# Kernel tuning notes

Hardware: AMD Instinct MI355X
Metric: run time of the kernel (lower is better)

Reference implementation:

```python
import jax, jax.numpy as jnp
import numpy as np

T, B, H, L = 200, 32, 1024, 2
DROPOUT = 0.32
KEEP = 1.0 - DROPOUT
FORGET_GATE_BIAS = 1.0


def setup_inputs() -> dict:
    key = jax.random.key(0)
    ks = jax.random.split(key, 8)
    scale = 1.0 / np.sqrt(H)  # torch LSTM default init: U(-1/sqrt(H), 1/sqrt(H))
    x = jax.random.normal(ks[0], (T, B, H), jnp.float32)
    W_ih = jax.random.uniform(ks[1], (L, 4 * H, H), jnp.float32, -scale, scale)
    W_hh = jax.random.uniform(ks[2], (L, 4 * H, H), jnp.float32, -scale, scale)
    b_ih = jax.random.uniform(ks[3], (L, 4 * H), jnp.float32, -scale, scale)
    b_hh = jax.random.uniform(ks[4], (L, 4 * H), jnp.float32, -scale, scale)
    # forget-gate bias init as in LstmDrop.__init__ (gate order i,f,g,o)
    b_ih = b_ih.at[:, H:2 * H].set(FORGET_GATE_BIAS)
    b_hh = b_hh.at[:, H:2 * H].set(0.0)
    h0 = jnp.zeros((L, B, H), jnp.float32)
    c0 = jnp.zeros((L, B, H), jnp.float32)
    # inverted dropout masks: inter-layer (torch LSTM dropout, applied to all but last layer)
    # and the trailing inplace Dropout on the output sequence
    mask_inter = (jax.random.bernoulli(ks[5], KEEP, (L - 1, T, B, H)) / KEEP).astype(jnp.float32)
    mask_out = (jax.random.bernoulli(ks[6], KEEP, (T, B, H)) / KEEP).astype(jnp.float32)
    return {"x": x, "h0": h0, "c0": c0, "W_ih": W_ih, "W_hh": W_hh,
            "b_ih": b_ih, "b_hh": b_hh, "mask_inter": mask_inter, "mask_out": mask_out}


def _lstm_layer(xs, h, c, Wih, Whh, b):
    # xs: [T,B,in]; Wih/Whh: [4H,in]/[4H,H]; b: [4H] (b_ih + b_hh fused)
    def step(carry, x_t):
        h, c = carry
        gates = x_t @ Wih.T + h @ Whh.T + b  # [B,4H]
        i, f, g, o = jnp.split(gates, 4, axis=-1)
        c = jax.nn.sigmoid(f) * c + jax.nn.sigmoid(i) * jnp.tanh(g)
        h = jax.nn.sigmoid(o) * jnp.tanh(c)
        return (h, c), h
    (hT, cT), ys = jax.lax.scan(step, (h, c), xs)
    return ys, hT, cT


def reference(x, h0, c0, W_ih, W_hh, b_ih, b_hh, mask_inter, mask_out):
    y = x
    h_last, c_last = [], []
    for l in range(L):
        y, hT, cT = _lstm_layer(y, h0[l], c0[l], W_ih[l], W_hh[l], b_ih[l] + b_hh[l])
        h_last.append(hT)
        c_last.append(cT)
        if l < L - 1:  # torch LSTM applies dropout between layers only
            y = y * mask_inter[l]
    y = y * mask_out  # the inplace Dropout on the output sequence
    return y, jnp.stack(h_last), jnp.stack(c_last)
```

## Files before the change

kernel.cpp:

```cpp
#include <hip/hip_runtime.h>

#define T_STEPS 200
#define BATCH   32
#define HID     1024
#define NWG     256
#define NTHR    512

typedef _Float16 half8 __attribute__((ext_vector_type(8)));
typedef float    f32x4 __attribute__((ext_vector_type(4)));

__device__ __forceinline__ half8 ld_coh16(const _Float16* p) {
    union { unsigned long long u[2]; half8 h; } r;
    const unsigned long long* q = (const unsigned long long*)p;
    r.u[0] = __hip_atomic_load(q,     __ATOMIC_RELAXED, __HIP_MEMORY_SCOPE_AGENT);
    r.u[1] = __hip_atomic_load(q + 1, __ATOMIC_RELAXED, __HIP_MEMORY_SCOPE_AGENT);
    return r.h;
}
__device__ __forceinline__ void st_coh16(_Float16* p, half8 v) {
    union { half8 h; unsigned long long u[2]; } r; r.h = v;
    unsigned long long* q = (unsigned long long*)p;
    __hip_atomic_store(q,     r.u[0], __ATOMIC_RELAXED, __HIP_MEMORY_SCOPE_AGENT);
    __hip_atomic_store(q + 1, r.u[1], __ATOMIC_RELAXED, __HIP_MEMORY_SCOPE_AGENT);
}

__device__ __forceinline__ half8 cvt8(const float* p) {
    f32x4 lo = *(const f32x4*)p;
    f32x4 hi = *(const f32x4*)(p + 4);
    half8 a;
    a[0] = (_Float16)lo[0]; a[1] = (_Float16)lo[1];
    a[2] = (_Float16)lo[2]; a[3] = (_Float16)lo[3];
    a[4] = (_Float16)hi[0]; a[5] = (_Float16)hi[1];
    a[6] = (_Float16)hi[2]; a[7] = (_Float16)hi[3];
    return a;
}

__global__ void init_k(const float* __restrict__ h0,
                       _Float16* __restrict__ h0b, _Float16* __restrict__ h1b,
                       unsigned* __restrict__ flag0, unsigned* __restrict__ flag1) {
    int i = blockIdx.x * blockDim.x + threadIdx.x;
    if (i < BATCH * HID) {
        h0b[i] = (_Float16)h0[i];
        h1b[i] = (_Float16)h0[BATCH * HID + i];
    }
    if (blockIdx.x == 0) {
        if (threadIdx.x < 128)      flag0[threadIdx.x * 32] = 0;
        else if (threadIdx.x < 256) flag1[(threadIdx.x - 128) * 32] = 0;
    }
}

__global__ __launch_bounds__(NTHR, 2) void lstm_main(
    const float* __restrict__ x, const float* __restrict__ c0,
    const float* __restrict__ Wih, const float* __restrict__ Whh,
    const float* __restrict__ bih, const float* __restrict__ bhh,
    const float* __restrict__ mi, const float* __restrict__ mo,
    float* __restrict__ out,
    _Float16* __restrict__ y0m, _Float16* __restrict__ h0b,
    _Float16* __restrict__ h1b, unsigned* __restrict__ flag0,
    unsigned* __restrict__ flag1)
{
    __shared__ _Float16 W_s[32 * 2048];
    __shared__ float scr[8][2][16][17];
    __shared__ float c_s[BATCH][8];
    __shared__ alignas(16) _Float16 st_h[BATCH][8];
    __shared__ alignas(16) _Float16 st_y[BATCH][8];
    __shared__ float st_o[BATCH][8];

    const int bid   = blockIdx.x;
    const int layer = bid >> 7;
    const int wgl   = bid & 127;
    const int tid   = threadIdx.x;

    const float* WihL = Wih + (size_t)layer * 4 * HID * HID;
    const float* WhhL = Whh + (size_t)layer * 4 * HID * HID;
    for (int idx = tid; idx < 32 * 2048; idx += NTHR) {
        int r = idx >> 11, k = idx & 2047;
        int grow = (r >> 3) * HID + wgl * 8 + (r & 7);
        float v = (k < HID) ? WihL[(size_t)grow * HID + k]
                            : WhhL[(size_t)grow * HID + (k - HID)];
        W_s[idx ^ ((r & 7) << 3)] = (_Float16)v;
    }

    float bias0 = 0.f, bias1 = 0.f, bias2 = 0.f, bias3 = 0.f;
    int b_ = 0, col_ = 0, gcol = 0;
    if (tid < 256) {
        b_ = tid >> 3; col_ = tid & 7; gcol = wgl * 8 + col_;
        bias0 = bih[layer * 4096 + gcol]           + bhh[layer * 4096 + gcol];
        bias1 = bih[layer * 4096 + HID + gcol]     + bhh[layer * 4096 + HID + gcol];
        bias2 = bih[layer * 4096 + 2 * HID + gcol] + bhh[layer * 4096 + 2 * HID + gcol];
        bias3 = bih[layer * 4096 + 3 * HID + gcol] + bhh[layer * 4096 + 3 * HID + gcol];
        c_s[b_][col_] = c0[((size_t)layer * BATCH + b_) * HID + gcol];
    }
    const int ot = tid - 256;
    const int b2 = (ot >= 0) ? (ot >> 3) : 0, c2 = (ot >= 0) ? (ot & 7) : 0;
    const int gcol2 = wgl * 8 + c2;
    __syncthreads();

    const int lane = tid & 63, wid = tid >> 6;
    int kq;
    if (layer == 0) kq = (wid < 4) ? (2 + (wid >> 1)) : ((wid - 4) >> 1);
    else            kq = wid >> 1;
    const int mm   = wid & 1;
    const int srow = kq * 2 + mm;
    const int row = lane & 15, bb = mm * 16 + row, ko = (lane >> 4) * 8;

    half8 aF[16];
    float mi_reg = 0.f, mo_reg = 0.f;
    if (layer == 0 && kq < 2) {
        const float* xp = x + (size_t)bb * HID + kq * 512 + ko;
        #pragma unroll
        for (int kk = 0; kk < 16; ++kk) aF[kk] = cvt8(xp + kk * 32);
    }
    if (layer == 1 && ot >= 0) mo_reg = mo[(size_t)b2 * HID + gcol2];

    for (int s = 0; s < T_STEPS; ++s) {
        if (layer == 0) {
            if (tid < 128) {
                const unsigned* f = flag0 + tid * 32;
                const unsigned tgt = (unsigned)s;
                while (__hip_atomic_load(f, __ATOMIC_RELAXED,
                                         __HIP_MEMORY_SCOPE_AGENT) < tgt) {}
            }
        } else {
            if (tid < 128) {
                const unsigned* f = flag0 + tid * 32;
                const unsigned tgt = (unsigned)(s + 1);
                while (__hip_atomic_load(f, __ATOMIC_RELAXED,
                                         __HIP_MEMORY_SCOPE_AGENT) < tgt) {}
            } else if (tid < 256) {
                const unsigned* f = flag1 + (tid - 128) * 32;
                const unsigned tgt = (unsigned)s;
                while (__hip_atomic_load(f, __ATOMIC_RELAXED,
                                         __HIP_MEMORY_SCOPE_AGENT) < tgt) {}
            }
        }
        asm volatile("" ::: "memory");
        __syncthreads();

        if (layer == 0 && tid < 256)
            mi_reg = mi[((size_t)s * BATCH + b_) * HID + gcol];

        if (layer == 0) {
            if (kq >= 2) {
                const _Float16* hp = h0b + (s & 1) * (BATCH * HID)
                                   + bb * HID + (kq - 2) * 512 + ko;
                #pragma unroll
                for (int kk = 0; kk < 16; ++kk) aF[kk] = ld_coh16(hp + kk * 32);
            }
        } else {
            if (kq < 2) {
                const _Float16* yp = y0m + ((size_t)s * BATCH + bb) * HID + kq * 512 + ko;
                #pragma unroll
                for (int kk = 0; kk < 16; ++kk) aF[kk] = ld_coh16(yp + kk * 32);
            } else {
                const _Float16* hp = h1b + (s & 1) * (BATCH * HID)
                                   + bb * HID + (kq - 2) * 512 + ko;
                #pragma unroll
                for (int kk = 0; kk < 16; ++kk) aF[kk] = ld_coh16(hp + kk * 32);
            }
        }

        f32x4 acc0 = {0.f, 0.f, 0.f, 0.f}, acc1 = {0.f, 0.f, 0.f, 0.f};
        #pragma unroll
        for (int kk = 0; kk < 16; ++kk) {
            const int k  = kq * 512 + kk * 32 + ko;
            const int r1 = 16 + row;
            const half8 bB0 = *(const half8*)&W_s[(row * 2048 + k) ^ ((row & 7) << 3)];
            const half8 bB1 = *(const half8*)&W_s[(r1 * 2048 + k) ^ ((r1 & 7) << 3)];
            acc0 = __builtin_amdgcn_mfma_f32_16x16x32_f16(aF[kk], bB0, acc0, 0, 0, 0);
            acc1 = __builtin_amdgcn_mfma_f32_16x16x32_f16(aF[kk], bB1, acc1, 0, 0, 0);
        }
        #pragma unroll
        for (int j = 0; j < 4; ++j) {
            scr[srow][0][(lane >> 4) * 4 + j][row] = acc0[j];
            scr[srow][1][(lane >> 4) * 4 + j][row] = acc1[j];
        }
        __syncthreads();

        if (tid < 256) {
            const int m2 = b_ >> 4, rD = b_ & 15;
            float v0 = 0.f, v1 = 0.f, v2 = 0.f, v3 = 0.f;
            #pragma unroll
            for (int q = 0; q < 4; ++q) {
                v0 += scr[q * 2 + m2][0][rD][col_];
                v1 += scr[q * 2 + m2][0][rD][8 + col_];
                v2 += scr[q * 2 + m2][1][rD][col_];
                v3 += scr[q * 2 + m2][1][rD][8 + col_];
            }
            const float ig = 1.f / (1.f + __expf(-(v0 + bias0)));
            const float fg = 1.f / (1.f + __expf(-(v1 + bias1)));
            const float gg = tanhf(v2 + bias2);
            const float og = 1.f / (1.f + __expf(-(v3 + bias3)));
            const float cc = fg * c_s[b_][col_] + ig * gg;
            const float hh = og * tanhf(cc);
            c_s[b_][col_] = cc;

            st_h[b_][col_] = (_Float16)hh;
            if (layer == 0) st_y[b_][col_] = (_Float16)(hh * mi_reg);
            else            st_o[b_][col_] = hh;

            if (s == T_STEPS - 1) {
                const size_t base = (size_t)T_STEPS * BATCH * HID;
                out[base + ((size_t)layer * BATCH + b_) * HID + gcol] = hh;
                out[base + (size_t)2 * BATCH * HID + ((size_t)layer * BATCH + b_) * HID + gcol] = cc;
            }
        }
        __syncthreads();

        if (layer == 0) {
            if (wid >= 4) {
                if (tid >= 448 && tid < 480) {
                    const int sl = tid - 448;
                    st_coh16(&h0b[((s + 1) & 1) * (BATCH * HID) + sl * HID + wgl * 8],
                             *(const half8*)st_h[sl]);
                    st_coh16(&y0m[((size_t)s * BATCH + sl) * HID + wgl * 8],
                             *(const half8*)st_y[sl]);
                    asm volatile("s_waitcnt vmcnt(0)" ::: "memory");
                    if (tid == 448)
                        __hip_atomic_store(flag0 + wgl * 32, (unsigned)(s + 1),
                                           __ATOMIC_RELAXED, __HIP_MEMORY_SCOPE_AGENT);
                }
                if (kq < 2 && s + 1 < T_STEPS) {
                    const float* xp = x + ((size_t)(s + 1) * BATCH + bb) * HID + kq * 512 + ko;
                    #pragma unroll
                    for (int kk = 0; kk < 16; ++kk) aF[kk] = cvt8(xp + kk * 32);
                }
            }
        } else {
            if (ot >= 0) {
                out[((size_t)s * BATCH + b2) * HID + gcol2] = st_o[b2][c2] * mo_reg;
                if (tid >= 448 && tid < 480) {
                    const int sl = tid - 448;
                    st_coh16(&h1b[((s + 1) & 1) * (BATCH * HID) + sl * HID + wgl * 8],
                             *(const half8*)st_h[sl]);
                    asm volatile("s_waitcnt vmcnt(0)" ::: "memory");
                    if (tid == 448)
                        __hip_atomic_store(flag1 + wgl * 32, (unsigned)(s + 1),
                                           __ATOMIC_RELAXED, __HIP_MEMORY_SCOPE_AGENT);
                }
                if (s + 1 < T_STEPS)
                    mo_reg = mo[((size_t)(s + 1) * BATCH + b2) * HID + gcol2];
            }
        }
    }
}

extern "C" void kernel_launch(void* const* d_in, const int* in_sizes, int n_in,
                              void* d_out, int out_size, void* d_ws, size_t ws_size,
                              hipStream_t stream) {
    const float* x   = (const float*)d_in[0];
    const float* h0  = (const float*)d_in[1];
    const float* c0  = (const float*)d_in[2];
    const float* Wih = (const float*)d_in[3];
    const float* Whh = (const float*)d_in[4];
    const float* bih = (const float*)d_in[5];
    const float* bhh = (const float*)d_in[6];
    const float* mi  = (const float*)d_in[7];
    const float* mo  = (const float*)d_in[8];
    float* out = (float*)d_out;

    char* w = (char*)d_ws;
    _Float16* y0m   = (_Float16*)w;
    _Float16* h0b   = (_Float16*)(w + 13107200);
    _Float16* h1b   = (_Float16*)(w + 13107200 + 131072);
    unsigned* flag0 = (unsigned*)(w + 13107200 + 262144);
    unsigned* flag1 = (unsigned*)(w + 13107200 + 262144 + 16384);

    hipLaunchKernelGGL(init_k, dim3(128), dim3(256), 0, stream,
                       h0, h0b, h1b, flag0, flag1);

    void* args[] = {(void*)&x, (void*)&c0, (void*)&Wih, (void*)&Whh,
                    (void*)&bih, (void*)&bhh, (void*)&mi, (void*)&mo,
                    (void*)&out, (void*)&y0m, (void*)&h0b, (void*)&h1b,
                    (void*)&flag0, (void*)&flag1};
    hipLaunchCooperativeKernel((void*)lstm_main, dim3(NWG), dim3(NTHR),
                               args, 0, stream);
}
```

Before: 2.170 ms.

## Replace per-step flag barriers with tagged hidden-state words for dataflow sync

```diff
diff --git a/kernel.cpp b/kernel.cpp
--- a/kernel.cpp
+++ b/kernel.cpp
@@ -5,22 +5,25 @@
 #define HID     1024
 #define NWG     256
 #define NTHR    512
+#define HB      (BATCH * HID)
 
 typedef _Float16 half8 __attribute__((ext_vector_type(8)));
 typedef float    f32x4 __attribute__((ext_vector_type(4)));
-
-__device__ __forceinline__ half8 ld_coh16(const _Float16* p) {
-    union { unsigned long long u[2]; half8 h; } r;
-    const unsigned long long* q = (const unsigned long long*)p;
-    r.u[0] = __hip_atomic_load(q,     __ATOMIC_RELAXED, __HIP_MEMORY_SCOPE_AGENT);
-    r.u[1] = __hip_atomic_load(q + 1, __ATOMIC_RELAXED, __HIP_MEMORY_SCOPE_AGENT);
-    return r.h;
-}
+typedef unsigned long long u64;
+
+#define RLX __ATOMIC_RELAXED
+#define AGT __HIP_MEMORY_SCOPE_AGENT
+#define TAGMASK 0xFFFF0000FFFF0000ull
+
+static __device__ __forceinline__ unsigned short f16bits(_Float16 v) {
+    union { _Float16 f; unsigned short u; } c; c.f = v; return c.u;
+}
+
 __device__ __forceinline__ void st_coh16(_Float16* p, half8 v) {
-    union { half8 h; unsigned long long u[2]; } r; r.h = v;
-    unsigned long long* q = (unsigned long long*)p;
-    __hip_atomic_store(q,     r.u[0], __ATOMIC_RELAXED, __HIP_MEMORY_SCOPE_AGENT);
-    __hip_atomic_store(q + 1, r.u[1], __ATOMIC_RELAXED, __HIP_MEMORY_SCOPE_AGENT);
+    union { half8 h; u64 u[2]; } r; r.h = v;
+    u64* q = (u64*)p;
+    __hip_atomic_store(q,     r.u[0], RLX, AGT);
+    __hip_atomic_store(q + 1, r.u[1], RLX, AGT);
 }
 
 __device__ __forceinline__ half8 cvt8(const float* p) {
@@ -35,17 +38,16 @@
 }
 
 __global__ void init_k(const float* __restrict__ h0,
-                       _Float16* __restrict__ h0b, _Float16* __restrict__ h1b,
-                       unsigned* __restrict__ flag0, unsigned* __restrict__ flag1) {
+                       unsigned* __restrict__ h0w, unsigned* __restrict__ h1w,
+                       unsigned* __restrict__ flag0) {
     int i = blockIdx.x * blockDim.x + threadIdx.x;
-    if (i < BATCH * HID) {
-        h0b[i] = (_Float16)h0[i];
-        h1b[i] = (_Float16)h0[BATCH * HID + i];
-    }
-    if (blockIdx.x == 0) {
-        if (threadIdx.x < 128)      flag0[threadIdx.x * 32] = 0;
-        else if (threadIdx.x < 256) flag1[(threadIdx.x - 128) * 32] = 0;
-    }
+    if (i < HB) {
+        h0w[i]      = (1u << 16) | f16bits((_Float16)h0[i]);
+        h0w[HB + i] = 0u;
+        h1w[i]      = (1u << 16) | f16bits((_Float16)h0[HB + i]);
+        h1w[HB + i] = 0u;
+    }
+    if (blockIdx.x == 0 && threadIdx.x < 128) flag0[threadIdx.x * 32] = 0u;
 }
 
 __global__ __launch_bounds__(NTHR, 2) void lstm_main(
@@ -54,15 +56,14 @@
     const float* __restrict__ bih, const float* __restrict__ bhh,
     const float* __restrict__ mi, const float* __restrict__ mo,
     float* __restrict__ out,
-    _Float16* __restrict__ y0m, _Float16* __restrict__ h0b,
-    _Float16* __restrict__ h1b, unsigned* __restrict__ flag0,
-    unsigned* __restrict__ flag1)
+    _Float16* __restrict__ y0m, unsigned* __restrict__ h0w,
+    unsigned* __restrict__ h1w, unsigned* __restrict__ flag0)
 {
     __shared__ _Float16 W_s[32 * 2048];
     __shared__ float scr[8][2][16][17];
     __shared__ float c_s[BATCH][8];
-    __shared__ alignas(16) _Float16 st_h[BATCH][8];
     __shared__ alignas(16) _Float16 st_y[BATCH][8];
+    __shared__ float st_mi[BATCH][8];
     __shared__ float st_o[BATCH][8];
 
     const int bid   = blockIdx.x;
@@ -93,6 +94,10 @@
     const int ot = tid - 256;
     const int b2 = (ot >= 0) ? (ot >> 3) : 0, c2 = (ot >= 0) ? (ot & 7) : 0;
     const int gcol2 = wgl * 8 + c2;
+
+    float mo_reg = 0.f;
+    if (layer == 0 && ot >= 0) st_mi[b2][c2] = mi[(size_t)b2 * HID + gcol2];
+    if (layer == 1 && ot >= 0) mo_reg = mo[(size_t)b2 * HID + gcol2];
     __syncthreads();
 
     const int lane = tid & 63, wid = tid >> 6;
@@ -104,71 +109,78 @@
     const int row = lane & 15, bb = mm * 16 + row, ko = (lane >> 4) * 8;
 
     half8 aF[16];
-    float mi_reg = 0.f, mo_reg = 0.f;
     if (layer == 0 && kq < 2) {
         const float* xp = x + (size_t)bb * HID + kq * 512 + ko;
         #pragma unroll
         for (int kk = 0; kk < 16; ++kk) aF[kk] = cvt8(xp + kk * 32);
     }
-    if (layer == 1 && ot >= 0) mo_reg = mo[(size_t)b2 * HID + gcol2];
 
     for (int s = 0; s < T_STEPS; ++s) {
-        if (layer == 0) {
-            if (tid < 128) {
-                const unsigned* f = flag0 + tid * 32;
-                const unsigned tgt = (unsigned)s;
-                while (__hip_atomic_load(f, __ATOMIC_RELAXED,
-                                         __HIP_MEMORY_SCOPE_AGENT) < tgt) {}
+        f32x4 acc0 = {0.f, 0.f, 0.f, 0.f}, acc1 = {0.f, 0.f, 0.f, 0.f};
+
+        if (kq >= 2) {
+            const unsigned* __restrict__ hsrc = (layer == 0) ? h0w : h1w;
+            const unsigned tg = (unsigned)(s + 1);
+            const u64 expect = ((u64)tg << 48) | ((u64)tg << 16);
+            const unsigned* basew = hsrc + (s & 1) * HB + bb * HID + (kq - 2) * 512 + ko;
+            #pragma unroll
+            for (int c = 0; c < 4; ++c) {
+                u64 w[16];
+                #pragma unroll
+                for (int i = 0; i < 16; ++i)
+                    w[i] = __hip_atomic_load(
+                        (const u64*)(basew + (c * 4 + (i >> 2)) * 32 + (i & 3) * 2), RLX, AGT);
+                for (;;) {
+                    u64 bad = 0;
+                    #pragma unroll
+                    for (int i = 0; i < 16; ++i) bad |= (w[i] & TAGMASK) ^ expect;
+                    if (__all(bad == 0)) break;
+                    #pragma unroll
+                    for (int i = 0; i < 16; ++i)
+                        w[i] = __hip_atomic_load(
+                            (const u64*)(basew + (c * 4 + (i >> 2)) * 32 + (i & 3) * 2), RLX, AGT);
+                }
+                #pragma unroll
+                for (int k2 = 0; k2 < 4; ++k2) {
+                    union { half8 h; unsigned short u[8]; } a;
+                    #pragma unroll
+                    for (int j = 0; j < 8; ++j)
+                        a.u[j] = (unsigned short)(w[k2 * 4 + (j >> 1)] >> (32 * (j & 1)));
+                    const int kk = c * 4 + k2;
+                    const int k  = kq * 512 + kk * 32 + ko;
+                    const int r1 = 16 + row;
+                    const half8 bB0 = *(const half8*)&W_s[(row * 2048 + k) ^ ((row & 7) << 3)];
+                    const half8 bB1 = *(const half8*)&W_s[(r1 * 2048 + k) ^ ((r1 & 7) << 3)];
+                    acc0 = __builtin_amdgcn_mfma_f32_16x16x32_f16(a.h, bB0, acc0, 0, 0, 0);
+                    acc1 = __builtin_amdgcn_mfma_f32_16x16x32_f16(a.h, bB1, acc1, 0, 0, 0);
+                }
             }
         } else {
-            if (tid < 128) {
-                const unsigned* f = flag0 + tid * 32;
+            if (layer == 1) {
                 const unsigned tgt = (unsigned)(s + 1);
-                while (__hip_atomic_load(f, __ATOMIC_RELAXED,
-                                         __HIP_MEMORY_SCOPE_AGENT) < tgt) {}
-            } else if (tid < 256) {
-                const unsigned* f = flag1 + (tid - 128) * 32;
-                const unsigned tgt = (unsigned)s;
-                while (__hip_atomic_load(f, __ATOMIC_RELAXED,
-                                         __HIP_MEMORY_SCOPE_AGENT) < tgt) {}
-            }
-        }
-        asm volatile("" ::: "memory");
-        __syncthreads();
-
-        if (layer == 0 && tid < 256)
-            mi_reg = mi[((size_t)s * BATCH + b_) * HID + gcol];
-
-        if (layer == 0) {
-            if (kq >= 2) {
-                const _Float16* hp = h0b + (s & 1) * (BATCH * HID)
-                                   + bb * HID + (kq - 2) * 512 + ko;
-                #pragma unroll
-                for (int kk = 0; kk < 16; ++kk) aF[kk] = ld_coh16(hp + kk * 32);
-            }
-        } else {
-            if (kq < 2) {
+                const unsigned* fa = flag0 + (lane * 2) * 32;
+                const unsigned* fb = flag0 + (lane * 2 + 1) * 32;
+                for (;;) {
+                    unsigned va = __hip_atomic_load(fa, RLX, AGT);
+                    unsigned vb = __hip_atomic_load(fb, RLX, AGT);
+                    if (__all((va >= tgt) & (vb >= tgt))) break;
+                }
+                asm volatile("" ::: "memory");
                 const _Float16* yp = y0m + ((size_t)s * BATCH + bb) * HID + kq * 512 + ko;
                 #pragma unroll
-                for (int kk = 0; kk < 16; ++kk) aF[kk] = ld_coh16(yp + kk * 32);
-            } else {
-                const _Float16* hp = h1b + (s & 1) * (BATCH * HID)
-                                   + bb * HID + (kq - 2) * 512 + ko;
-                #pragma unroll
-                for (int kk = 0; kk < 16; ++kk) aF[kk] = ld_coh16(hp + kk * 32);
-            }
-        }
-
-        f32x4 acc0 = {0.f, 0.f, 0.f, 0.f}, acc1 = {0.f, 0.f, 0.f, 0.f};
-        #pragma unroll
-        for (int kk = 0; kk < 16; ++kk) {
-            const int k  = kq * 512 + kk * 32 + ko;
-            const int r1 = 16 + row;
-            const half8 bB0 = *(const half8*)&W_s[(row * 2048 + k) ^ ((row & 7) << 3)];
-            const half8 bB1 = *(const half8*)&W_s[(r1 * 2048 + k) ^ ((r1 & 7) << 3)];
-            acc0 = __builtin_amdgcn_mfma_f32_16x16x32_f16(aF[kk], bB0, acc0, 0, 0, 0);
-            acc1 = __builtin_amdgcn_mfma_f32_16x16x32_f16(aF[kk], bB1, acc1, 0, 0, 0);
-        }
+                for (int kk = 0; kk < 16; ++kk) aF[kk] = *(const half8*)(yp + kk * 32);
+            }
+            #pragma unroll
+            for (int kk = 0; kk < 16; ++kk) {
+                const int k  = kq * 512 + kk * 32 + ko;
+                const int r1 = 16 + row;
+                const half8 bB0 = *(const half8*)&W_s[(row * 2048 + k) ^ ((row & 7) << 3)];
+                const half8 bB1 = *(const half8*)&W_s[(r1 * 2048 + k) ^ ((r1 & 7) << 3)];
+                acc0 = __builtin_amdgcn_mfma_f32_16x16x32_f16(aF[kk], bB0, acc0, 0, 0, 0);
+                acc1 = __builtin_amdgcn_mfma_f32_16x16x32_f16(aF[kk], bB1, acc1, 0, 0, 0);
+            }
+        }
+
         #pragma unroll
         for (int j = 0; j < 4; ++j) {
             scr[srow][0][(lane >> 4) * 4 + j][row] = acc0[j];
@@ -194,49 +206,45 @@
             const float hh = og * tanhf(cc);
             c_s[b_][col_] = cc;
 
-            st_h[b_][col_] = (_Float16)hh;
-            if (layer == 0) st_y[b_][col_] = (_Float16)(hh * mi_reg);
-            else            st_o[b_][col_] = hh;
-
+            const unsigned hwrd = ((unsigned)(s + 2) << 16)
+                                | (unsigned)f16bits((_Float16)hh);
+            if (layer == 0) {
+                __hip_atomic_store(h0w + ((s + 1) & 1) * HB + b_ * HID + gcol,
+                                   hwrd, RLX, AGT);
+                st_y[b_][col_] = (_Float16)(hh * st_mi[b_][col_]);
+            } else {
+                __hip_atomic_store(h1w + ((s + 1) & 1) * HB + b_ * HID + gcol,
+                                   hwrd, RLX, AGT);
+                st_o[b_][col_] = hh;
+            }
             if (s == T_STEPS - 1) {
                 const size_t base = (size_t)T_STEPS * BATCH * HID;
                 out[base + ((size_t)layer * BATCH + b_) * HID + gcol] = hh;
-                out[base + (size_t)2 * BATCH * HID + ((size_t)layer * BATCH + b_) * HID + gcol] = cc;
+                out[base + (size_t)2 * BATCH * HID
+                    + ((size_t)layer * BATCH + b_) * HID + gcol] = cc;
             }
         }
         __syncthreads();
 
         if (layer == 0) {
-            if (wid >= 4) {
-                if (tid >= 448 && tid < 480) {
-                    const int sl = tid - 448;
-                    st_coh16(&h0b[((s + 1) & 1) * (BATCH * HID) + sl * HID + wgl * 8],
-                             *(const half8*)st_h[sl]);
-                    st_coh16(&y0m[((size_t)s * BATCH + sl) * HID + wgl * 8],
-                             *(const half8*)st_y[sl]);
-                    asm volatile("s_waitcnt vmcnt(0)" ::: "memory");
-                    if (tid == 448)
-                        __hip_atomic_store(flag0 + wgl * 32, (unsigned)(s + 1),
-                                           __ATOMIC_RELAXED, __HIP_MEMORY_SCOPE_AGENT);
-                }
-                if (kq < 2 && s + 1 < T_STEPS) {
-                    const float* xp = x + ((size_t)(s + 1) * BATCH + bb) * HID + kq * 512 + ko;
-                    #pragma unroll
-                    for (int kk = 0; kk < 16; ++kk) aF[kk] = cvt8(xp + kk * 32);
-                }
+            if (tid >= 448 && tid < 480) {
+                const int sl = tid - 448;
+                st_coh16(&y0m[((size_t)s * BATCH + sl) * HID + wgl * 8],
+                         *(const half8*)st_y[sl]);
+                asm volatile("s_waitcnt vmcnt(0)" ::: "memory");
+                if (tid == 448)
+                    __hip_atomic_store(flag0 + wgl * 32, (unsigned)(s + 1), RLX, AGT);
+            }
+            if (ot >= 0 && s + 1 < T_STEPS)
+                st_mi[b2][c2] = mi[((size_t)(s + 1) * BATCH + b2) * HID + gcol2];
+            if (wid >= 4 && kq < 2 && s + 1 < T_STEPS) {
+                const float* xp = x + ((size_t)(s + 1) * BATCH + bb) * HID + kq * 512 + ko;
+                #pragma unroll
+                for (int kk = 0; kk < 16; ++kk) aF[kk] = cvt8(xp + kk * 32);
             }
         } else {
             if (ot >= 0) {
                 out[((size_t)s * BATCH + b2) * HID + gcol2] = st_o[b2][c2] * mo_reg;
-                if (tid >= 448 && tid < 480) {
-                    const int sl = tid - 448;
-                    st_coh16(&h1b[((s + 1) & 1) * (BATCH * HID) + sl * HID + wgl * 8],
-                             *(const half8*)st_h[sl]);
-                    asm volatile("s_waitcnt vmcnt(0)" ::: "memory");
-                    if (tid == 448)
-                        __hip_atomic_store(flag1 + wgl * 32, (unsigned)(s + 1),
-                                           __ATOMIC_RELAXED, __HIP_MEMORY_SCOPE_AGENT);
-                }
                 if (s + 1 < T_STEPS)
                     mo_reg = mo[((size_t)(s + 1) * BATCH + b2) * HID + gcol2];
             }
@@ -260,18 +268,16 @@
 
     char* w = (char*)d_ws;
     _Float16* y0m   = (_Float16*)w;
-    _Float16* h0b   = (_Float16*)(w + 13107200);
-    _Float16* h1b   = (_Float16*)(w + 13107200 + 131072);
-    unsigned* flag0 = (unsigned*)(w + 13107200 + 262144);
-    unsigned* flag1 = (unsigned*)(w + 13107200 + 262144 + 16384);
-
-    hipLaunchKernelGGL(init_k, dim3(128), dim3(256), 0, stream,
-                       h0, h0b, h1b, flag0, flag1);
+    unsigned* h0w   = (unsigned*)(w + 13107200);
+    unsigned* h1w   = (unsigned*)(w + 13107200 + 262144);
+    unsigned* flag0 = (unsigned*)(w + 13107200 + 524288);
+
+    hipLaunchKernelGGL(init_k, dim3(128), dim3(256), 0, stream, h0, h0w, h1w, flag0);
 
     void* args[] = {(void*)&x, (void*)&c0, (void*)&Wih, (void*)&Whh,
                     (void*)&bih, (void*)&bhh, (void*)&mi, (void*)&mo,
-                    (void*)&out, (void*)&y0m, (void*)&h0b, (void*)&h1b,
-                    (void*)&flag0, (void*)&flag1};
+                    (void*)&out, (void*)&y0m, (void*)&h0w, (void*)&h1w,
+                    (void*)&flag0};
     hipLaunchCooperativeKernel((void*)lstm_main, dim3(NWG), dim3(NTHR),
                                args, 0, stream);
 }
```

Measured after the change: 2.817 ms. +29.8%, slower.
